# Kernel optimization log

Hardware: AMD Instinct MI355X
Metric: run time of the kernel (lower is better)

Reference implementation:

```python
import jax, jax.numpy as jnp
import numpy as np

NUM_HEADS = 16
DIM_HEAD = 64
SCALE = DIM_HEAD ** -0.5
ROPE_BASE = 10000.0


def _rope(t):
    # t: [b, h, n, d] -> rotary embedding with rotate-half convention
    n, d = t.shape[2], t.shape[3]
    inv_freq = 1.0 / (ROPE_BASE ** (jnp.arange(0, d, 2, dtype=jnp.float32) / d))
    freqs = jnp.arange(n, dtype=jnp.float32)[:, None] * inv_freq[None, :]  # [n, d/2]
    cos = jnp.concatenate([jnp.cos(freqs), jnp.cos(freqs)], axis=-1)  # [n, d]
    sin = jnp.concatenate([jnp.sin(freqs), jnp.sin(freqs)], axis=-1)
    t1, t2 = jnp.split(t, 2, axis=-1)
    rot = jnp.concatenate([-t2, t1], axis=-1)
    return t * cos + rot * sin


def setup_inputs() -> dict:
    key = jax.random.key(0)
    k1, k2, k3 = jax.random.split(key, 3)
    B, N, D = 2, 2049, 1024  # 2048 patches + 1 cls token
    x = jax.random.normal(k1, (B, N, D), dtype=jnp.float32)
    ln_gamma = jnp.ones((D,), dtype=jnp.float32)
    ln_beta = jnp.zeros((D,), dtype=jnp.float32)
    w_qkv = jax.random.normal(k2, (D, 3 * NUM_HEADS * DIM_HEAD), dtype=jnp.float32) * 0.02
    w_out = jax.random.normal(k3, (NUM_HEADS * DIM_HEAD, D), dtype=jnp.float32) * 0.02
    return {"x": x, "ln_gamma": ln_gamma, "ln_beta": ln_beta, "w_qkv": w_qkv, "w_out": w_out}


def reference(x, ln_gamma, ln_beta, w_qkv, w_out):
    B, N, D = x.shape
    # LayerNorm (eps=1e-5, torch default)
    mu = jnp.mean(x, axis=-1, keepdims=True)
    var = jnp.mean(jnp.square(x - mu), axis=-1, keepdims=True)
    xn = (x - mu) * jax.lax.rsqrt(var + 1e-5) * ln_gamma + ln_beta
    # QKV projection (no bias)
    qkv = xn @ w_qkv  # [B, N, 3*H*Dh]
    q, k, v = jnp.split(qkv, 3, axis=-1)
    def to_heads(t):
        return t.reshape(B, N, NUM_HEADS, DIM_HEAD).transpose(0, 2, 1, 3)  # [B,H,N,Dh]
    q, k, v = to_heads(q), to_heads(k), to_heads(v)
    # cls token excluded from RoPE
    q = jnp.concatenate([q[:, :, :1, :], _rope(q[:, :, 1:, :])], axis=2)
    k = jnp.concatenate([k[:, :, :1, :], _rope(k[:, :, 1:, :])], axis=2)
    dots = jnp.einsum('bhqd,bhkd->bhqk', q, k) * SCALE
    attn = jax.nn.softmax(dots, axis=-1)
    out = jnp.einsum('bhqk,bhkd->bhqd', attn, v)
    out = out.transpose(0, 2, 1, 3).reshape(B, N, NUM_HEADS * DIM_HEAD)
    return out @ w_out
```

## Files before the change

### kernel.cpp

```cpp
#include <hip/hip_runtime.h>

#define B_    2
#define N_    2049
#define NPAD  2112
#define D_    1024
#define H_    16
#define DH    64
#define MROWS (B_ * N_)
#define MPAD  4224
#define QSCALE 0.18033688011117674f

using bf16x8 = __attribute__((ext_vector_type(8))) short;
using f32x4  = __attribute__((ext_vector_type(4))) float;
using f32x16 = __attribute__((ext_vector_type(16))) float;

#define AS1 __attribute__((address_space(1)))
#define AS3 __attribute__((address_space(3)))

__device__ __forceinline__ float bf2f(short s) {
  union { unsigned u; float f; } a; a.u = ((unsigned)(unsigned short)s) << 16; return a.f;
}
__device__ __forceinline__ short f2bf(float f) {
  union { float f; unsigned u; } a; a.f = f;
  unsigned r = a.u + 0x7fffu + ((a.u >> 16) & 1u);
  return (short)(r >> 16);
}
__device__ __forceinline__ float hexp2(float x) { return __builtin_amdgcn_exp2f(x); }
__device__ __forceinline__ void dma16(const short* g, AS3 short* l) {
  __builtin_amdgcn_global_load_lds((const AS1 unsigned*)g, (AS3 unsigned*)l, 16, 0, 0);
}

__device__ __forceinline__ size_t tiled_off(int m, int k) {
  return ((size_t)(m >> 7) << 17)
       + (size_t)(((k >> 5) << 12)
       + ((((m & 127) >> 4)) << 9)
       + (((((m & 15) << 2) | ((k & 31) >> 3))) << 3)
       + (k & 7));
}

__global__ __launch_bounds__(256) void prep_kernel(const float* __restrict__ x,
                                                   const float* __restrict__ gamma,
                                                   const float* __restrict__ beta,
                                                   short* __restrict__ xn,
                                                   const float* __restrict__ w_qkv,
                                                   short* __restrict__ wqkvT,
                                                   const float* __restrict__ w_out,
                                                   short* __restrict__ woutT) {
  int blk = blockIdx.x;
  int tid = threadIdx.x;
  __shared__ float T[64][65];
  __shared__ float sb[4], s2b[4];

  if (blk < MROWS) {
    int row = blk;
    int b = row >= N_;
    int rowp = b * NPAD + (row - b * N_);
    const float4 v = ((const float4*)(x + (size_t)row * D_))[tid];
    float s  = v.x + v.y + v.z + v.w;
    float ss = v.x * v.x + v.y * v.y + v.z * v.z + v.w * v.w;
    for (int o = 1; o < 64; o <<= 1) { s += __shfl_xor(s, o, 64); ss += __shfl_xor(ss, o, 64); }
    int wid = tid >> 6;
    if ((tid & 63) == 0) { sb[wid] = s; s2b[wid] = ss; }
    __syncthreads();
    float st  = sb[0] + sb[1] + sb[2] + sb[3];
    float sst = s2b[0] + s2b[1] + s2b[2] + s2b[3];
    float mu  = st * (1.0f / D_);
    float var = sst * (1.0f / D_) - mu * mu;
    float rs  = rsqrtf(var + 1e-5f);
    const float4 g  = ((const float4*)gamma)[tid];
    const float4 be = ((const float4*)beta)[tid];
    short4 o4;
    o4.x = f2bf((v.x - mu) * rs * g.x + be.x);
    o4.y = f2bf((v.y - mu) * rs * g.y + be.y);
    o4.z = f2bf((v.z - mu) * rs * g.z + be.z);
    o4.w = f2bf((v.w - mu) * rs * g.w + be.w);
    *(short4*)(xn + tiled_off(rowp, tid * 4)) = o4;
    return;
  }

  const float* in; short* out; int Nn, t2;
  int b2 = blk - MROWS;
  if (b2 < 768) { in = w_qkv; out = wqkvT; Nn = 3072; t2 = b2; }
  else          { in = w_out; out = woutT; Nn = 1024; t2 = b2 - 768; }
  int k0 = (t2 & 15) * 64;
  int n0 = (t2 >> 4) * 64;
  int r = tid >> 2, c0 = (tid & 3) * 16;
  const float* ip = in + (size_t)(k0 + r) * Nn + n0 + c0;
  #pragma unroll
  for (int j = 0; j < 4; ++j) {
    float4 v = *(const float4*)(ip + j * 4);
    T[r][c0 + j * 4 + 0] = v.x; T[r][c0 + j * 4 + 1] = v.y;
    T[r][c0 + j * 4 + 2] = v.z; T[r][c0 + j * 4 + 3] = v.w;
  }
  __syncthreads();
  bf16x8 w0, w1;
  #pragma unroll
  for (int j = 0; j < 8; ++j) {
    w0[j] = f2bf(T[c0 + j][r]);
    w1[j] = f2bf(T[c0 + 8 + j][r]);
  }
  *(bf16x8*)(out + tiled_off(n0 + r, k0 + c0))     = w0;
  *(bf16x8*)(out + tiled_off(n0 + r, k0 + c0 + 8)) = w1;
}

#define BM 128
#define BK 32
__global__ __launch_bounds__(256) void gemm_qkv_rope(const short* __restrict__ A,
                                                     const short* __restrict__ BT,
                                                     short* __restrict__ qg,
                                                     short* __restrict__ kfrag,
                                                     short* __restrict__ vfrag) {
  int lane = threadIdx.x & 63, wid = threadIdx.x >> 6;
  int quad = lane >> 4, l16 = lane & 15;
  int wr = wid >> 1, wc = wid & 1;
  int chunk = gridDim.x >> 3;
  int swz = (blockIdx.x & 7) * chunk + (blockIdx.x >> 3);
  int mb = swz % 33, nb = swz / 33;
  int m0 = mb * BM;
  int n0 = nb * BM;

  __shared__ __align__(16) short pool[17408];
  AS3 short* AbufL = (AS3 short*)pool;
  AS3 short* BbufL = (AS3 short*)(pool + 8192);
  const short* AbufR = pool;
  const short* BbufR = pool + 8192;

  f32x4 acc[4][4] = {};

  const short* Ap = A  + ((size_t)(m0 >> 7) << 17);
  const short* Bp = BT + ((size_t)(n0 >> 7) << 17);

  auto stage = [&](int kt, int bb) {
    #pragma unroll
    for (int i = 0; i < 2; ++i) {
      int j = wid * 2 + i;
      dma16(Ap + ((size_t)kt << 12) + j * 512 + lane * 8, AbufL + bb * 4096 + j * 512);
      dma16(Bp + ((size_t)kt << 12) + j * 512 + lane * 8, BbufL + bb * 4096 + j * 512);
    }
  };

  stage(0, 0);
  __syncthreads();

  for (int kt = 0; kt < 32; ++kt) {
    int cur = kt & 1;
    if (kt + 1 < 32) stage(kt + 1, cur ^ 1);
    const short* Ab = AbufR + cur * 4096;
    const short* Bb = BbufR + cur * 4096;
    bf16x8 af[4], bfr[4];
    #pragma unroll
    for (int s = 0; s < 4; ++s)
      af[s] = *(const bf16x8*)&Ab[(wr * 64 + s * 16 + l16) * BK + quad * 8];
    #pragma unroll
    for (int t = 0; t < 4; ++t)
      bfr[t] = *(const bf16x8*)&Bb[(wc * 64 + t * 16 + l16) * BK + quad * 8];
    #pragma unroll
    for (int s = 0; s < 4; ++s)
      #pragma unroll
      for (int t = 0; t < 4; ++t)
        acc[s][t] = __builtin_amdgcn_mfma_f32_16x16x32_bf16(af[s], bfr[t], acc[s][t], 0, 0, 0);
    __syncthreads();
  }

  short* Ct = pool;
  #pragma unroll
  for (int s = 0; s < 4; ++s)
    #pragma unroll
    for (int t = 0; t < 4; ++t) {
      int col = wc * 64 + t * 16 + l16;
      #pragma unroll
      for (int r = 0; r < 4; ++r) {
        int row = wr * 64 + s * 16 + quad * 4 + r;
        Ct[row * 136 + col] = f2bf(acc[s][t][r]);
      }
    }
  __syncthreads();

  int third = nb >> 3;
  int hpair = (nb & 7) * 2;
  int tid = threadIdx.x;

  if (third == 0) {
    int p = tid & 3, nl = tid >> 2;
    #pragma unroll
    for (int tt = 0; tt < 2; ++tt) {
      int rl = tt * 64 + nl;
      int rg = m0 + rl;
      int b = rg >= NPAD;
      int n = rg - b * NPAD;
      bool valid = n < N_;
      bool rot = valid && n > 0;
      float csv[8], snv[8];
      #pragma unroll
      for (int j = 0; j < 8; ++j) {
        int i = p * 8 + j;
        float ang = rot ? (float)(n - 1) * hexp2((float)i * -0.4152410118609203f) : 0.0f;
        float rev = ang * 0.15915494309189535f;
        rev = rev - floorf(rev);
        snv[j] = rot ? __builtin_amdgcn_sinf(rev) : 0.0f;
        csv[j] = rot ? __builtin_amdgcn_cosf(rev) : 1.0f;
      }
      #pragma unroll
      for (int hh = 0; hh < 2; ++hh) {
        bf16x8 w1v = {}, w2v = {};
        if (valid) {
          bf16x8 va = *(const bf16x8*)&Ct[rl * 136 + hh * 64 + p * 8];
          bf16x8 vb = *(const bf16x8*)&Ct[rl * 136 + hh * 64 + p * 8 + 32];
          #pragma unroll
          for (int j = 0; j < 8; ++j) {
            float a = bf2f(va[j]), b2 = bf2f(vb[j]);
            w1v[j] = f2bf((a * csv[j] - b2 * snv[j]) * QSCALE);
            w2v[j] = f2bf((b2 * csv[j] + a * snv[j]) * QSCALE);
          }
        }
        size_t ob = ((size_t)(b * 16 + hpair + hh) * NPAD + n) * DH;
        *(bf16x8*)(qg + ob + p * 8)      = w1v;
        *(bf16x8*)(qg + ob + 32 + p * 8) = w2v;
      }
    }
  } else if (third == 1) {
    int rl = tid & 127, hi = tid >> 7;
    int rg = m0 + rl;
    int b = rg >= NPAD;
    int n = rg - b * NPAD;
    bool valid = n < N_;
    bool rot = valid && n > 0;
    int kt = n >> 6, g = (n >> 5) & 1, lk = n & 31;
    int l = hi * 32 + lk;
    #pragma unroll
    for (int s2 = 0; s2 < 2; ++s2) {
      float csv[8], snv[8];
      #pragma unroll
      for (int j = 0; j < 8; ++j) {
        int i = s2 * 16 + hi * 8 + j;
        float ang = rot ? (float)(n - 1) * hexp2((float)i * -0.4152410118609203f) : 0.0f;
        float rev = ang * 0.15915494309189535f;
        rev = rev - floorf(rev);
        snv[j] = rot ? __builtin_amdgcn_sinf(rev) : 0.0f;
        csv[j] = rot ? __builtin_amdgcn_cosf(rev) : 1.0f;
      }
      #pragma unroll
      for (int hh = 0; hh < 2; ++hh) {
        bf16x8 wlo = {}, whi = {};
        if (valid) {
          bf16x8 va = *(const bf16x8*)&Ct[rl * 136 + hh * 64 + s2 * 16 + hi * 8];
          bf16x8 vb = *(const bf16x8*)&Ct[rl * 136 + hh * 64 + s2 * 16 + hi * 8 + 32];
          #pragma unroll
          for (int j = 0; j < 8; ++j) {
            float a = bf2f(va[j]), b2 = bf2f(vb[j]);
            wlo[j] = f2bf(a * csv[j] - b2 * snv[j]);
            whi[j] = f2bf(b2 * csv[j] + a * snv[j]);
          }
        }
        short* base = kfrag + (size_t)(b * 16 + hpair + hh) * NPAD * DH + (size_t)kt * 4096;
        *(bf16x8*)(base + (g * 4 + s2) * 512 + l * 8)     = wlo;
        *(bf16x8*)(base + (g * 4 + s2 + 2) * 512 + l * 8) = whi;
      }
    }
  } else {
    int lk = tid & 31, z = tid >> 5;
    #pragma unroll
    for (int oo = 0; oo < 2; ++oo) {
      int o = z * 2 + oo;
      int rg = m0 + o * 8;
      int b = rg >= NPAD;
      int n0o = rg - b * NPAD;
      int kt = n0o >> 6;
      int s = (n0o >> 4) & 3;
      int hi = (n0o >> 3) & 1;
      #pragma unroll
      for (int hh = 0; hh < 2; ++hh) {
        short* base = vfrag + (size_t)(b * 16 + hpair + hh) * NPAD * DH + (size_t)kt * 4096;
        #pragma unroll
        for (int m = 0; m < 2; ++m) {
          bf16x8 wv = {};
          #pragma unroll
          for (int j = 0; j < 8; ++j)
            if (n0o + j < N_) wv[j] = Ct[(o * 8 + j) * 136 + hh * 64 + m * 32 + lk];
          *(bf16x8*)(base + (m * 4 + s) * 512 + (hi * 32 + lk) * 8) = wv;
        }
      }
    }
  }
}

__global__ __launch_bounds__(256) void gemm_out(const short* __restrict__ A,
                                                const short* __restrict__ BT,
                                                float* __restrict__ C) {
  int lane = threadIdx.x & 63, wid = threadIdx.x >> 6;
  int quad = lane >> 4, l16 = lane & 15;
  int wr = wid >> 1, wc = wid & 1;
  int chunk = gridDim.x >> 3;
  int swz = (blockIdx.x & 7) * chunk + (blockIdx.x >> 3);
  int mb = swz % 66, nb = swz / 66;
  int m0 = mb * 64;
  int n0 = nb * 128;

  __shared__ __align__(16) short Abuf[2][2048];
  __shared__ __align__(16) short Bbuf[2][4096];
  AS3 short* AbufL = (AS3 short*)&Abuf[0][0];
  AS3 short* BbufL = (AS3 short*)&Bbuf[0][0];

  f32x4 acc[2][4] = {};

  const short* Ap = A  + ((size_t)(m0 >> 7) << 17);
  const short* Bp = BT + ((size_t)(n0 >> 7) << 17);
  int jbA = (m0 & 127) >> 4;

  auto stage = [&](int kt, int bb) {
    dma16(Ap + ((size_t)kt << 12) + (jbA + wid) * 512 + lane * 8, AbufL + bb * 2048 + wid * 512);
    #pragma unroll
    for (int i = 0; i < 2; ++i) {
      int j = wid * 2 + i;
      dma16(Bp + ((size_t)kt << 12) + j * 512 + lane * 8, BbufL + bb * 4096 + j * 512);
    }
  };

  stage(0, 0);
  __syncthreads();

  for (int kt = 0; kt < 32; ++kt) {
    int cur = kt & 1;
    if (kt + 1 < 32) stage(kt + 1, cur ^ 1);
    const short* Ab = &Abuf[cur][0];
    const short* Bb = &Bbuf[cur][0];
    bf16x8 af[2], bfr[4];
    #pragma unroll
    for (int s = 0; s < 2; ++s)
      af[s] = *(const bf16x8*)&Ab[(wr * 32 + s * 16 + l16) * BK + quad * 8];
    #pragma unroll
    for (int t = 0; t < 4; ++t)
      bfr[t] = *(const bf16x8*)&Bb[(wc * 64 + t * 16 + l16) * BK + quad * 8];
    #pragma unroll
    for (int s = 0; s < 2; ++s)
      #pragma unroll
      for (int t = 0; t < 4; ++t)
        acc[s][t] = __builtin_amdgcn_mfma_f32_16x16x32_bf16(af[s], bfr[t], acc[s][t], 0, 0, 0);
    __syncthreads();
  }

  #pragma unroll
  for (int s = 0; s < 2; ++s)
    #pragma unroll
    for (int r = 0; r < 4; ++r) {
      int row = m0 + wr * 32 + s * 16 + quad * 4 + r;
      if (row < MROWS) {
        size_t rb = (size_t)row * 1024 + n0 + wc * 64;
        #pragma unroll
        for (int t = 0; t < 4; ++t)
          C[rb + t * 16 + l16] = acc[s][t][r];
      }
    }
}

__global__ __launch_bounds__(256, 3) void attn_kernel(const short* __restrict__ qg,
                                                      const short* __restrict__ kfrag,
                                                      const short* __restrict__ vfrag,
                                                      short* __restrict__ out) {
  int blk = blockIdx.x;
  int xcd = blk & 7;
  int t_  = blk >> 3;
  int bh  = xcd * 4 + (t_ & 3);
  int qblk = t_ >> 2;
  int b = bh >> 4, h = bh & 15;

  int lane = threadIdx.x & 63, wid = threadIdx.x >> 6;
  int q    = lane & 31;
  int half = lane >> 5;
  int q0   = qblk * 128 + wid * 32;
  size_t hb = (size_t)bh * NPAD * DH;
  const short* kf_hb = kfrag + hb;
  const short* vf_hb = vfrag + hb;

  __shared__ __align__(16) short Kbuf[3][4096];
  __shared__ __align__(16) short Vbuf[3][4096];
  AS3 short* KbufL = (AS3 short*)&Kbuf[0][0];
  AS3 short* VbufL = (AS3 short*)&Vbuf[0][0];
  const short* KbufR = &Kbuf[0][0];
  const short* VbufR = &Vbuf[0][0];

  int qr = q0 + q; if (qr >= NPAD) qr = 0;
  const short* qp = qg + hb + (size_t)qr * DH + half * 8;
  bf16x8 qf[4];
  #pragma unroll
  for (int s = 0; s < 4; ++s) qf[s] = *(const bf16x8*)(qp + s * 16);

  f32x16 o0 = {}, o1 = {};
  float lrun = 0.0f;

  auto stage = [&](int kt, int bb) {
    const short* ksrc = kf_hb + (size_t)kt * 4096;
    const short* vsrc = vf_hb + (size_t)kt * 4096;
    #pragma unroll
    for (int i = 0; i < 2; ++i) {
      int j = wid * 2 + i;
      dma16(ksrc + j * 512 + lane * 8, KbufL + bb * 4096 + j * 512);
      dma16(vsrc + j * 512 + lane * 8, VbufL + bb * 4096 + j * 512);
    }
  };

  stage(0, 0);
  stage(1, 1);

  #define NKT 33
  for (int kt = 0; kt < NKT; ++kt) {
    int rb = kt % 3;
    int k0 = kt * 64;

    if (kt == NKT - 1) asm volatile("s_waitcnt vmcnt(0)" ::: "memory");
    else               asm volatile("s_waitcnt vmcnt(4)" ::: "memory");
    __builtin_amdgcn_s_barrier();

    if (kt + 2 < NKT) stage(kt + 2, (kt + 2) % 3);
    __builtin_amdgcn_sched_barrier(0);

    const short* Vc = VbufR + rb * 4096;
    bf16x8 vf0[4], vf1[4];
    #pragma unroll
    for (int s = 0; s < 4; ++s) {
      vf0[s] = *(const bf16x8*)&Vc[(0 * 4 + s) * 512 + lane * 8];
      vf1[s] = *(const bf16x8*)&Vc[(4 + s) * 512 + lane * 8];
    }

    const short* Kc = KbufR + rb * 4096;
    f32x16 sA = {}, sB = {};
    __builtin_amdgcn_s_setprio(1);
    #pragma unroll
    for (int s = 0; s < 4; ++s) {
      bf16x8 kf0 = *(const bf16x8*)&Kc[(0 * 4 + s) * 512 + lane * 8];
      bf16x8 kf1 = *(const bf16x8*)&Kc[(1 * 4 + s) * 512 + lane * 8];
      sA = __builtin_amdgcn_mfma_f32_32x32x16_bf16(kf0, qf[s], sA, 0, 0, 0);
      sB = __builtin_amdgcn_mfma_f32_32x32x16_bf16(kf1, qf[s], sB, 0, 0, 0);
    }
    __builtin_amdgcn_s_setprio(0);

    if (k0 + 64 > N_) {
      #pragma unroll
      for (int rr = 0; rr < 16; ++rr) {
        int key = (rr & 3) + 8 * (rr >> 2) + 4 * half;
        if (k0 + key >= N_)      sA[rr] = -1e30f;
        if (k0 + 32 + key >= N_) sB[rr] = -1e30f;
      }
    }

    float vsum = 0.0f;
    #pragma unroll
    for (int rr = 0; rr < 16; ++rr) {
      sA[rr] = hexp2(sA[rr]); vsum += sA[rr];
      sB[rr] = hexp2(sB[rr]); vsum += sB[rr];
    }
    lrun += vsum;

    unsigned w[4][4];
    #pragma unroll
    for (int g = 0; g < 2; ++g) {
      #pragma unroll
      for (int fs = 0; fs < 2; ++fs) {
        int b0 = fs * 8;
        float e0, e1, e2, e3, e4, e5, e6, e7;
        if (g == 0) {
          e0 = sA[b0+0]; e1 = sA[b0+1]; e2 = sA[b0+2]; e3 = sA[b0+3];
          e4 = sA[b0+4]; e5 = sA[b0+5]; e6 = sA[b0+6]; e7 = sA[b0+7];
        } else {
          e0 = sB[b0+0]; e1 = sB[b0+1]; e2 = sB[b0+2]; e3 = sB[b0+3];
          e4 = sB[b0+4]; e5 = sB[b0+5]; e6 = sB[b0+6]; e7 = sB[b0+7];
        }
        unsigned X1, X2, Y1, Y2;
        asm("v_cvt_pk_bf16_f32 %0, %1, %2" : "=v"(X1) : "v"(e0), "v"(e1));
        asm("v_cvt_pk_bf16_f32 %0, %1, %2" : "=v"(X2) : "v"(e2), "v"(e3));
        asm("v_cvt_pk_bf16_f32 %0, %1, %2" : "=v"(Y1) : "v"(e4), "v"(e5));
        asm("v_cvt_pk_bf16_f32 %0, %1, %2" : "=v"(Y2) : "v"(e6), "v"(e7));
        asm("v_permlane32_swap_b32 %0, %1" : "+v"(X1), "+v"(Y1));
        asm("v_permlane32_swap_b32 %0, %1" : "+v"(X2), "+v"(Y2));
        int kst = g * 2 + fs;
        w[kst][0] = X1; w[kst][1] = X2; w[kst][2] = Y1; w[kst][3] = Y2;
      }
    }

    __builtin_amdgcn_s_setprio(1);
    #pragma unroll
    for (int kst = 0; kst < 4; ++kst) {
      union { unsigned u[4]; bf16x8 v; } bw;
      bw.u[0] = w[kst][0]; bw.u[1] = w[kst][1]; bw.u[2] = w[kst][2]; bw.u[3] = w[kst][3];
      o0 = __builtin_amdgcn_mfma_f32_32x32x16_bf16(vf0[kst], bw.v, o0, 0, 0, 0);
      o1 = __builtin_amdgcn_mfma_f32_32x32x16_bf16(vf1[kst], bw.v, o1, 0, 0, 0);
    }
    __builtin_amdgcn_s_setprio(0);
  }

  lrun += __shfl_xor(lrun, 32, 64);

  int qrow = q0 + q;
  if (qrow < N_) {
    float inv = 1.0f / lrun;
    int grow = b * N_ + qrow;
    #pragma unroll
    for (int m = 0; m < 2; ++m) {
      #pragma unroll
      for (int gq = 0; gq < 4; ++gq) {
        float a0 = (m ? o1[gq*4+0] : o0[gq*4+0]) * inv;
        float a1 = (m ? o1[gq*4+1] : o0[gq*4+1]) * inv;
        float a2 = (m ? o1[gq*4+2] : o0[gq*4+2]) * inv;
        float a3 = (m ? o1[gq*4+3] : o0[gq*4+3]) * inv;
        short4 st;
        st.x = f2bf(a0); st.y = f2bf(a1); st.z = f2bf(a2); st.w = f2bf(a3);
        int dh = m * 32 + gq * 8 + half * 4;
        *(short4*)(out + tiled_off(grow, h * DH + dh)) = st;
      }
    }
  }
}

extern "C" void kernel_launch(void* const* d_in, const int* in_sizes, int n_in,
                              void* d_out, int out_size, void* d_ws, size_t ws_size,
                              hipStream_t stream) {
  const float* x     = (const float*)d_in[0];
  const float* gamma = (const float*)d_in[1];
  const float* beta  = (const float*)d_in[2];
  const float* w_qkv = (const float*)d_in[3];
  const float* w_out = (const float*)d_in[4];

  short* wqkvT = (short*)d_ws;
  short* woutT = wqkvT + (size_t)3072 * 1024;
  short* xn    = woutT + (size_t)1024 * 1024;
  short* qg    = xn    + (size_t)MPAD * 1024;
  short* kfragG = qg    + (size_t)B_ * H_ * NPAD * DH;
  short* vfragG = kfragG + (size_t)B_ * H_ * NPAD * DH;
  short* attn_out = xn;

  prep_kernel<<<MROWS + 768 + 256, 256, 0, stream>>>(x, gamma, beta, xn,
                                                     w_qkv, wqkvT, w_out, woutT);
  gemm_qkv_rope<<<792, 256, 0, stream>>>(xn, wqkvT, qg, kfragG, vfragG);
  attn_kernel<<<544, 256, 0, stream>>>(qg, kfragG, vfragG, attn_out);
  gemm_out<<<528, 256, 0, stream>>>(attn_out, woutT, (float*)d_out);
}
```

Baseline: 212.7 us.

## Software-pipeline attention loop so QK of next tile overlaps PV of previous

```diff
diff --git a/kernel.cpp b/kernel.cpp
--- a/kernel.cpp
+++ b/kernel.cpp
@@ -9,6 +9,7 @@
 #define MROWS (B_ * N_)
 #define MPAD  4224
 #define QSCALE 0.18033688011117674f
+#define NKT   33
 
 using bf16x8 = __attribute__((ext_vector_type(8))) short;
 using f32x4  = __attribute__((ext_vector_type(4))) float;
@@ -373,7 +374,7 @@
   const short* vf_hb = vfrag + hb;
 
   __shared__ __align__(16) short Kbuf[3][4096];
-  __shared__ __align__(16) short Vbuf[3][4096];
+  __shared__ __align__(16) short Vbuf[4][4096];
   AS3 short* KbufL = (AS3 short*)&Kbuf[0][0];
   AS3 short* VbufL = (AS3 short*)&Vbuf[0][0];
   const short* KbufR = &Kbuf[0][0];
@@ -388,41 +389,32 @@
   f32x16 o0 = {}, o1 = {};
   float lrun = 0.0f;
 
-  auto stage = [&](int kt, int bb) {
+  auto stage = [&](int kt) {
     const short* ksrc = kf_hb + (size_t)kt * 4096;
     const short* vsrc = vf_hb + (size_t)kt * 4096;
     #pragma unroll
     for (int i = 0; i < 2; ++i) {
       int j = wid * 2 + i;
-      dma16(ksrc + j * 512 + lane * 8, KbufL + bb * 4096 + j * 512);
-      dma16(vsrc + j * 512 + lane * 8, VbufL + bb * 4096 + j * 512);
+      dma16(ksrc + j * 512 + lane * 8, KbufL + (kt % 3) * 4096 + j * 512);
+      dma16(vsrc + j * 512 + lane * 8, VbufL + (kt & 3) * 4096 + j * 512);
     }
   };
 
-  stage(0, 0);
-  stage(1, 1);
-
-  #define NKT 33
-  for (int kt = 0; kt < NKT; ++kt) {
-    int rb = kt % 3;
+  stage(0);
+  stage(1);
+
+  unsigned wA[4][4], wB[4][4];
+
+  auto qkpart = [&](int kt, unsigned (&wc)[4][4]) {
     int k0 = kt * 64;
-
     if (kt == NKT - 1) asm volatile("s_waitcnt vmcnt(0)" ::: "memory");
     else               asm volatile("s_waitcnt vmcnt(4)" ::: "memory");
     __builtin_amdgcn_s_barrier();
 
-    if (kt + 2 < NKT) stage(kt + 2, (kt + 2) % 3);
+    if (kt + 2 < NKT) stage(kt + 2);
     __builtin_amdgcn_sched_barrier(0);
 
-    const short* Vc = VbufR + rb * 4096;
-    bf16x8 vf0[4], vf1[4];
-    #pragma unroll
-    for (int s = 0; s < 4; ++s) {
-      vf0[s] = *(const bf16x8*)&Vc[(0 * 4 + s) * 512 + lane * 8];
-      vf1[s] = *(const bf16x8*)&Vc[(4 + s) * 512 + lane * 8];
-    }
-
-    const short* Kc = KbufR + rb * 4096;
+    const short* Kc = KbufR + (kt % 3) * 4096;
     f32x16 sA = {}, sB = {};
     __builtin_amdgcn_s_setprio(1);
     #pragma unroll
@@ -451,7 +443,6 @@
     }
     lrun += vsum;
 
-    unsigned w[4][4];
     #pragma unroll
     for (int g = 0; g < 2; ++g) {
       #pragma unroll
@@ -473,20 +464,39 @@
         asm("v_permlane32_swap_b32 %0, %1" : "+v"(X1), "+v"(Y1));
         asm("v_permlane32_swap_b32 %0, %1" : "+v"(X2), "+v"(Y2));
         int kst = g * 2 + fs;
-        w[kst][0] = X1; w[kst][1] = X2; w[kst][2] = Y1; w[kst][3] = Y2;
-      }
-    }
-
+        wc[kst][0] = X1; wc[kst][1] = X2; wc[kst][2] = Y1; wc[kst][3] = Y2;
+      }
+    }
+  };
+
+  auto pvpart = [&](int kt, unsigned (&wp)[4][4]) {
+    const short* Vc = VbufR + (kt & 3) * 4096;
+    bf16x8 vf0[4], vf1[4];
+    #pragma unroll
+    for (int s = 0; s < 4; ++s) {
+      vf0[s] = *(const bf16x8*)&Vc[(0 * 4 + s) * 512 + lane * 8];
+      vf1[s] = *(const bf16x8*)&Vc[(4 + s) * 512 + lane * 8];
+    }
     __builtin_amdgcn_s_setprio(1);
     #pragma unroll
     for (int kst = 0; kst < 4; ++kst) {
       union { unsigned u[4]; bf16x8 v; } bw;
-      bw.u[0] = w[kst][0]; bw.u[1] = w[kst][1]; bw.u[2] = w[kst][2]; bw.u[3] = w[kst][3];
+      bw.u[0] = wp[kst][0]; bw.u[1] = wp[kst][1]; bw.u[2] = wp[kst][2]; bw.u[3] = wp[kst][3];
       o0 = __builtin_amdgcn_mfma_f32_32x32x16_bf16(vf0[kst], bw.v, o0, 0, 0, 0);
       o1 = __builtin_amdgcn_mfma_f32_32x32x16_bf16(vf1[kst], bw.v, o1, 0, 0, 0);
     }
     __builtin_amdgcn_s_setprio(0);
-  }
+  };
+
+  qkpart(0, wA);
+  #pragma unroll 1
+  for (int i = 0; i < 16; ++i) {
+    qkpart(2 * i + 1, wB);
+    pvpart(2 * i,     wA);
+    qkpart(2 * i + 2, wA);
+    pvpart(2 * i + 1, wB);
+  }
+  pvpart(32, wA);
 
   lrun += __shfl_xor(lrun, 32, 64);
 
```

New measurement: 225.6 us. 1.06x slower.
